# Performance work log

Measured on AMD Instinct MI355X. Metric: run time of the kernel, lower is better.

The kernel has to match this reference:

```python
import jax, jax.numpy as jnp
import numpy as np

H = W = 2048
TANH_C = 1.1486328125  # probability-correction constant from the model
DEG2RAD = np.float32(np.pi / 180.0)

# Fire-spread direction angle (degrees, East=0, counterclockwise) from the
# neighbor at 3x3 window position (r, c) toward the center cell.
DIR_DEG = jnp.array([[315., 270., 225.],
                     [  0.,   0., 180.],
                     [ 45.,  90., 135.]], dtype=jnp.float32)
CENTER_MASK = jnp.ones((3, 3), jnp.float32).at[1, 1].set(0.0)  # exclude self


def _neighborhood(x):
    """x: [H,W] -> [H,W,3,3] with [i,j,r,c] = x[i+r-1, j+c-1], zero padded."""
    xp = jnp.pad(x, 1)
    return jnp.stack(
        [jnp.stack([xp[r:r + H, c:c + W] for c in range(3)], axis=-1)
         for r in range(3)], axis=-2)


def setup_inputs() -> dict:
    key = jax.random.key(0)
    ks = jax.random.split(key, 8)
    p_veg = jax.random.uniform(ks[0], (H, W), jnp.float32)
    p_den = jax.random.uniform(ks[1], (H, W), jnp.float32)
    wind_velocity = jax.random.uniform(ks[2], (H, W), jnp.float32) * 10.0
    wind_towards_direction = jax.random.uniform(ks[3], (H, W), jnp.float32) * 360.0
    slope = (jax.random.uniform(ks[4], (H, W, 3, 3), jnp.float32) - 0.5) * 60.0
    burning = jax.random.uniform(ks[5], (H, W)) < 0.01  # sparse initial ignition
    burned = jnp.zeros((H, W), dtype=bool)
    rand_ignite = jax.random.uniform(ks[6], (H, W), jnp.float32)
    rand_continue = jax.random.uniform(ks[7], (H, W), jnp.float32)
    return dict(
        p_veg=p_veg, p_den=p_den,
        wind_velocity=wind_velocity, wind_towards_direction=wind_towards_direction,
        slope=slope,
        a=jnp.float32(0.1), p_h=jnp.float32(0.3),
        c_1=jnp.float32(0.1), c_2=jnp.float32(0.1), p_continue=jnp.float32(0.3),
        rand_ignite=rand_ignite, rand_continue=rand_continue,
        burning=burning, burned=burned,
    )


def reference(p_veg, p_den, wind_velocity, wind_towards_direction, slope,
              a, p_h, c_1, c_2, p_continue,
              rand_ignite, rand_continue, burning, burned):
    # p_w = exp(c1*V) * exp(c2*V*(cos(theta_w)-1)), theta_w = angle between
    # wind direction and per-neighbor spread direction. [H,W,3,3]
    theta_w = (wind_towards_direction[..., None, None] - DIR_DEG) * DEG2RAD
    p_w = (jnp.exp(c_1 * wind_velocity)[..., None, None]
           * jnp.exp(c_2 * wind_velocity[..., None, None] * (jnp.cos(theta_w) - 1.0)))
    # p_s = exp(a * theta_s), slope angle in radians. [H,W,3,3]
    p_s = jnp.exp(a * slope * DEG2RAD)
    # p_propagate = tanh(c * p_h*(1+p_veg)*(1+p_den)*p_w*p_s)
    p_base = p_h * (1.0 + p_veg) * (1.0 + p_den)  # [H,W]
    p_prop = jnp.tanh(TANH_C * (p_base[..., None, None] * p_w * p_s))
    # 8-neighbor burning indicators (center masked out). [H,W,3,3]
    nbr_burning = _neighborhood(burning.astype(jnp.float32)) * CENTER_MASK
    # p_ignite = 1 - prod_j (1 - p_propagate_j * burning_j)
    p_ignite = 1.0 - jnp.prod(1.0 - p_prop * nbr_burning, axis=(-2, -1))
    # Stochastic state transition.
    burnable = ~burning & ~burned
    new_ignited = burnable & (rand_ignite < p_ignite)
    keep = burning & (rand_continue < p_continue)
    new_burning = new_ignited | keep
    new_burned = burned | (burning & ~keep)
    return p_ignite, jnp.stack([new_burning, new_burned])
```

## Files before the change

kernel.cpp:

```cpp
#include <hip/hip_runtime.h>
#include <math.h>

namespace {

constexpr int H = 2048;
constexpr int W = 2048;
constexpr int HW = H * W;
constexpr float TANH_C  = 1.1486328125f;
constexpr float DEG2RAD = 0.017453292519943295f;
constexpr float RT2H    = 0.70710678118654752f;
constexpr float LOG2E   = 1.4426950408889634f;
constexpr float TWOPI   = 6.283185307179586f;

__device__ __forceinline__ float fexp2(float x) {
#if __has_builtin(__builtin_amdgcn_exp2f)
    return __builtin_amdgcn_exp2f(x);
#else
    return __exp2f(x);
#endif
}
__device__ __forceinline__ float fcos_rev(float x) {
#if __has_builtin(__builtin_amdgcn_cosf)
    return __builtin_amdgcn_cosf(x);
#else
    return __cosf(x * TWOPI);
#endif
}
__device__ __forceinline__ float fsin_rev(float x) {
#if __has_builtin(__builtin_amdgcn_sinf)
    return __builtin_amdgcn_sinf(x);
#else
    return __sinf(x * TWOPI);
#endif
}
__device__ __forceinline__ float frcp(float x) {
#if __has_builtin(__builtin_amdgcn_rcpf)
    return __builtin_amdgcn_rcpf(x);
#else
    return 1.0f / x;
#endif
}

__global__ __launch_bounds__(256) void wildfire_step(
    const float* __restrict__ p_veg,  const float* __restrict__ p_den,
    const float* __restrict__ wind_v, const float* __restrict__ wind_d,
    const float* __restrict__ slope,
    const float* __restrict__ s_a,  const float* __restrict__ s_ph,
    const float* __restrict__ s_c1, const float* __restrict__ s_c2,
    const float* __restrict__ s_pc,
    const float* __restrict__ rand_ig, const float* __restrict__ rand_co,
    const int* __restrict__ burning, const int* __restrict__ burned,
    float* __restrict__ out)
{
    __shared__ __align__(16) float sb[3][1032];
    __shared__ __align__(16) float pig_lds[1024];
    __shared__ unsigned short q[1024];
    __shared__ int qn;

    const int t  = (int)threadIdx.x;
    const int i  = (int)blockIdx.y;
    const int j0 = (int)blockIdx.x * 1024;
    const int rowbase = i * W + j0;

    if (t == 0) qn = 0;

    for (int r = 0; r < 3; ++r) {
        const int ii = i + r - 1;
        const bool rowok = (ii >= 0) && (ii < H);
        int4 v = make_int4(0, 0, 0, 0);
        if (rowok)
            v = *reinterpret_cast<const int4*>(burning + ii * W + j0 + 4 * t);
        float4 f;
        f.x = v.x ? 1.f : 0.f;  f.y = v.y ? 1.f : 0.f;
        f.z = v.z ? 1.f : 0.f;  f.w = v.w ? 1.f : 0.f;
        *reinterpret_cast<float4*>(&sb[r][4 + 4 * t]) = f;
        if (t == 0)
            sb[r][3] = (rowok && j0 > 0) ?
                       (burning[ii * W + j0 - 1] ? 1.f : 0.f) : 0.f;
        if (t == 1)
            sb[r][4 + 1024] = (rowok && j0 + 1024 < W) ?
                       (burning[ii * W + j0 + 1024] ? 1.f : 0.f) : 0.f;
    }
    __syncthreads();

    const int jb = t * 4;
    const int idx = rowbase + jb;

    float r0[6], r1[6], r2[6];
    {
        const float4 a = *reinterpret_cast<const float4*>(&sb[0][4 + jb]);
        const float4 b = *reinterpret_cast<const float4*>(&sb[1][4 + jb]);
        const float4 c = *reinterpret_cast<const float4*>(&sb[2][4 + jb]);
        r0[0] = sb[0][3 + jb]; r0[1] = a.x; r0[2] = a.y; r0[3] = a.z; r0[4] = a.w; r0[5] = sb[0][8 + jb];
        r1[0] = sb[1][3 + jb]; r1[1] = b.x; r1[2] = b.y; r1[3] = b.z; r1[4] = b.w; r1[5] = sb[1][8 + jb];
        r2[0] = sb[2][3 + jb]; r2[1] = c.x; r2[2] = c.y; r2[3] = c.z; r2[4] = c.w; r2[5] = sb[2][8 + jb];
    }

    float anyn[4];
    bool  isb[4];
#pragma unroll
    for (int x = 0; x < 4; ++x) {
        anyn[x] = ((r0[x] + r0[x+1]) + (r0[x+2] + r1[x]))
                + ((r1[x+2] + r2[x]) + (r2[x+1] + r2[x+2]));
        isb[x]  = (r1[x+1] != 0.f);
        if (anyn[x] != 0.f) {
            const int pos = atomicAdd(&qn, 1);
            q[pos] = (unsigned short)(jb + x);
        }
    }
    *reinterpret_cast<float4*>(&pig_lds[jb]) = make_float4(0.f, 0.f, 0.f, 0.f);
    __syncthreads();

    const int n = qn;
    for (int k = t; k < n; k += 256) {
        const int cell = (int)q[k];
        const int c    = 4 + cell;
        const float b0 = sb[0][c-1], b1 = sb[0][c], b2 = sb[0][c+1];
        const float b3 = sb[1][c-1],                b5 = sb[1][c+1];
        const float b6 = sb[2][c-1], b7 = sb[2][c], b8 = sb[2][c+1];
        const float cnt = ((b0 + b1) + (b2 + b3)) + ((b5 + b6) + (b7 + b8));

        const int gidx = rowbase + cell;
        const float pv = p_veg[gidx];
        const float pd = p_den[gidx];
        const float wv = wind_v[gidx];
        const float wd = wind_d[gidx];
        float sl[9];
        __builtin_memcpy(sl, slope + (size_t)gidx * 9, 9 * sizeof(float));

        const float a_  = s_a[0];
        const float p_h = s_ph[0];
        const float c1  = s_c1[0];
        const float c2  = s_c2[0];

        const float wrev = wd * (1.f / 360.f);
        const float cw = fcos_rev(wrev);
        const float sw = fsin_rev(wrev);

        const float Lc2wv = (LOG2E * c2) * wv;
        const float cwv = Lc2wv * cw, swv = Lc2wv * sw;
        const float cwr = RT2H * cwv, swr = RT2H * swv;
        const float dpl = cwr + swr;
        const float dmi = cwr - swr;
        const float aslL = (a_ * DEG2RAD) * LOG2E;
        const float p_base = (p_h * (1.f + pv)) * (1.f + pd);
        const float Cz2 = (2.f * LOG2E * TANH_C) * p_base
                        * fexp2(LOG2E * (c1 * wv - c2 * wv));

#define NEIGHBOR(K, b, T, sv)                                            \
        const float q##K = fmaf(aslL, (sv), (T));                        \
        const float z##K = Cz2 * fexp2(q##K);                            \
        const float E##K = fexp2(z##K);                                  \
        const float d##K = fmaf((b), E##K, 1.f);

        NEIGHBOR(0, b0,  dmi, sl[0])
        NEIGHBOR(1, b1, -swv, sl[1])
        NEIGHBOR(2, b2, -dpl, sl[2])
        NEIGHBOR(3, b3,  cwv, sl[3])
        NEIGHBOR(5, b5, -cwv, sl[5])
        NEIGHBOR(6, b6,  dpl, sl[6])
        NEIGHBOR(7, b7,  swv, sl[7])
        NEIGHBOR(8, b8, -dmi, sl[8])
#undef NEIGHBOR
        const float den = ((d0 * d1) * (d2 * d3)) * ((d5 * d6) * (d7 * d8));
        const float num = fexp2(cnt);
        pig_lds[cell] = fmaf(-num, frcp(den), 1.f);
    }
    __syncthreads();

    const int4  burned4 = *reinterpret_cast<const int4*>(burned + idx);
    const int   bn[4]   = {burned4.x, burned4.y, burned4.z, burned4.w};
    const float p_cont  = s_pc[0];

    const float4 pig4 = *reinterpret_cast<const float4*>(&pig_lds[jb]);
    const float pig[4] = {pig4.x, pig4.y, pig4.z, pig4.w};

    float rc[4] = {1.f, 1.f, 1.f, 1.f};
    if (isb[0] || isb[1] || isb[2] || isb[3]) {
        const float4 rco4 = *reinterpret_cast<const float4*>(rand_co + idx);
        rc[0] = rco4.x; rc[1] = rco4.y; rc[2] = rco4.z; rc[3] = rco4.w;
    }
    float rig[4] = {1.f, 1.f, 1.f, 1.f};
    if ((anyn[0] + anyn[1]) + (anyn[2] + anyn[3]) != 0.f) {
        const float4 rig4 = *reinterpret_cast<const float4*>(rand_ig + idx);
        rig[0] = rig4.x; rig[1] = rig4.y; rig[2] = rig4.z; rig[3] = rig4.w;
    }

    float4 o0, o1, o2;
    float* o0p = &o0.x; float* o1p = &o1.x; float* o2p = &o2.x;
#pragma unroll
    for (int x = 0; x < 4; ++x) {
        const bool ni   = (!isb[x]) && (bn[x] == 0) && (rig[x] < pig[x]);
        const bool keep = isb[x] && (rc[x] < p_cont);
        const bool nb   = ni || keep;
        const bool nd   = (bn[x] != 0) || (isb[x] && !keep);
        o0p[x] = pig[x];
        o1p[x] = nb ? 1.f : 0.f;
        o2p[x] = nd ? 1.f : 0.f;
    }
    *reinterpret_cast<float4*>(out + idx)          = o0;
    *reinterpret_cast<float4*>(out + HW + idx)     = o1;
    *reinterpret_cast<float4*>(out + 2 * HW + idx) = o2;
}

}

extern "C" void kernel_launch(void* const* d_in, const int* in_sizes, int n_in,
                              void* d_out, int out_size, void* d_ws, size_t ws_size,
                              hipStream_t stream)
{
    (void)in_sizes; (void)n_in; (void)out_size; (void)d_ws; (void)ws_size;
    dim3 grid(W / 1024, H, 1);
    dim3 block(256, 1, 1);
    hipLaunchKernelGGL(wildfire_step, grid, block, 0, stream,
        (const float*)d_in[0],  (const float*)d_in[1],
        (const float*)d_in[2],  (const float*)d_in[3],
        (const float*)d_in[4],
        (const float*)d_in[5],  (const float*)d_in[6],
        (const float*)d_in[7],  (const float*)d_in[8],
        (const float*)d_in[9],
        (const float*)d_in[10], (const float*)d_in[11],
        (const int*)d_in[12],   (const int*)d_in[13],
        (float*)d_out);
}
```

Baseline: 305.2 us.

## Split into dense state-transition kernel and sparse heavy ignition kernel

Splits the single kernel into two launches. A dense elementwise kernel writes zero p_ignite, the keep flag and the burned state for every cell. A second kernel recomputes the burning neighbourhood, evaluates the probability only for cells with burning neighbours and scatters p_ignite and new-ignition flags directly. This drops the LDS staging buffer and the extra barrier in the heavy path, but unconditionally reads rand_continue and writes all outputs twice for the affected cells, and it adds a second launch.

```diff
diff --git a/kernel.cpp b/kernel.cpp
--- a/kernel.cpp
+++ b/kernel.cpp
@@ -41,19 +41,47 @@
 #endif
 }
 
-__global__ __launch_bounds__(256) void wildfire_step(
+__global__ __launch_bounds__(256) void wildfire_dense(
+    const float* __restrict__ rand_co,
+    const int* __restrict__ burning, const int* __restrict__ burned,
+    const float* __restrict__ s_pc,
+    float* __restrict__ out)
+{
+    const int idx = ((int)blockIdx.x * 256 + (int)threadIdx.x) * 4;
+    const int4   b4  = *reinterpret_cast<const int4*>(burning + idx);
+    const int4   bd4 = *reinterpret_cast<const int4*>(burned + idx);
+    const float4 rc4 = *reinterpret_cast<const float4*>(rand_co + idx);
+    const float  p_cont = s_pc[0];
+
+    const int   bn[4] = {b4.x, b4.y, b4.z, b4.w};
+    const int   bd[4] = {bd4.x, bd4.y, bd4.z, bd4.w};
+    const float rc[4] = {rc4.x, rc4.y, rc4.z, rc4.w};
+
+    float4 o1, o2;
+    float* o1p = &o1.x; float* o2p = &o2.x;
+#pragma unroll
+    for (int x = 0; x < 4; ++x) {
+        const bool isb  = (bn[x] != 0);
+        const bool keep = isb && (rc[x] < p_cont);
+        o1p[x] = keep ? 1.f : 0.f;
+        o2p[x] = ((bd[x] != 0) || (isb && !keep)) ? 1.f : 0.f;
+    }
+    *reinterpret_cast<float4*>(out + idx)          = make_float4(0.f, 0.f, 0.f, 0.f);
+    *reinterpret_cast<float4*>(out + HW + idx)     = o1;
+    *reinterpret_cast<float4*>(out + 2 * HW + idx) = o2;
+}
+
+__global__ __launch_bounds__(256) void wildfire_heavy(
     const float* __restrict__ p_veg,  const float* __restrict__ p_den,
     const float* __restrict__ wind_v, const float* __restrict__ wind_d,
     const float* __restrict__ slope,
     const float* __restrict__ s_a,  const float* __restrict__ s_ph,
     const float* __restrict__ s_c1, const float* __restrict__ s_c2,
-    const float* __restrict__ s_pc,
-    const float* __restrict__ rand_ig, const float* __restrict__ rand_co,
+    const float* __restrict__ rand_ig,
     const int* __restrict__ burning, const int* __restrict__ burned,
     float* __restrict__ out)
 {
     __shared__ __align__(16) float sb[3][1032];
-    __shared__ __align__(16) float pig_lds[1024];
     __shared__ unsigned short q[1024];
     __shared__ int qn;
 
@@ -84,54 +112,50 @@
     __syncthreads();
 
     const int jb = t * 4;
-    const int idx = rowbase + jb;
-
-    float r0[6], r1[6], r2[6];
     {
         const float4 a = *reinterpret_cast<const float4*>(&sb[0][4 + jb]);
         const float4 b = *reinterpret_cast<const float4*>(&sb[1][4 + jb]);
         const float4 c = *reinterpret_cast<const float4*>(&sb[2][4 + jb]);
-        r0[0] = sb[0][3 + jb]; r0[1] = a.x; r0[2] = a.y; r0[3] = a.z; r0[4] = a.w; r0[5] = sb[0][8 + jb];
-        r1[0] = sb[1][3 + jb]; r1[1] = b.x; r1[2] = b.y; r1[3] = b.z; r1[4] = b.w; r1[5] = sb[1][8 + jb];
-        r2[0] = sb[2][3 + jb]; r2[1] = c.x; r2[2] = c.y; r2[3] = c.z; r2[4] = c.w; r2[5] = sb[2][8 + jb];
-    }
-
-    float anyn[4];
-    bool  isb[4];
+        const float r0[6] = {sb[0][3 + jb], a.x, a.y, a.z, a.w, sb[0][8 + jb]};
+        const float r1[6] = {sb[1][3 + jb], b.x, b.y, b.z, b.w, sb[1][8 + jb]};
+        const float r2[6] = {sb[2][3 + jb], c.x, c.y, c.z, c.w, sb[2][8 + jb]};
 #pragma unroll
-    for (int x = 0; x < 4; ++x) {
-        anyn[x] = ((r0[x] + r0[x+1]) + (r0[x+2] + r1[x]))
-                + ((r1[x+2] + r2[x]) + (r2[x+1] + r2[x+2]));
-        isb[x]  = (r1[x+1] != 0.f);
-        if (anyn[x] != 0.f) {
-            const int pos = atomicAdd(&qn, 1);
-            q[pos] = (unsigned short)(jb + x);
+        for (int x = 0; x < 4; ++x) {
+            const float anyn = ((r0[x] + r0[x+1]) + (r0[x+2] + r1[x]))
+                             + ((r1[x+2] + r2[x]) + (r2[x+1] + r2[x+2]));
+            if (anyn != 0.f) {
+                const int pos = atomicAdd(&qn, 1);
+                q[pos] = (unsigned short)(jb + x);
+            }
         }
     }
-    *reinterpret_cast<float4*>(&pig_lds[jb]) = make_float4(0.f, 0.f, 0.f, 0.f);
     __syncthreads();
 
     const int n = qn;
+    const float a_  = s_a[0];
+    const float p_h = s_ph[0];
+    const float c1  = s_c1[0];
+    const float c2  = s_c2[0];
+    const float aslL = (a_ * DEG2RAD) * LOG2E;
+
     for (int k = t; k < n; k += 256) {
         const int cell = (int)q[k];
         const int c    = 4 + cell;
+        const int gidx = rowbase + cell;
+
+        const float pv  = p_veg[gidx];
+        const float pd  = p_den[gidx];
+        const float wv  = wind_v[gidx];
+        const float wd  = wind_d[gidx];
+        const float rig = rand_ig[gidx];
+        const int   bn  = burned[gidx];
+        float sl[9];
+        __builtin_memcpy(sl, slope + (size_t)gidx * 9, 9 * sizeof(float));
+
         const float b0 = sb[0][c-1], b1 = sb[0][c], b2 = sb[0][c+1];
-        const float b3 = sb[1][c-1],                b5 = sb[1][c+1];
+        const float b3 = sb[1][c-1], bcn = sb[1][c], b5 = sb[1][c+1];
         const float b6 = sb[2][c-1], b7 = sb[2][c], b8 = sb[2][c+1];
         const float cnt = ((b0 + b1) + (b2 + b3)) + ((b5 + b6) + (b7 + b8));
-
-        const int gidx = rowbase + cell;
-        const float pv = p_veg[gidx];
-        const float pd = p_den[gidx];
-        const float wv = wind_v[gidx];
-        const float wd = wind_d[gidx];
-        float sl[9];
-        __builtin_memcpy(sl, slope + (size_t)gidx * 9, 9 * sizeof(float));
-
-        const float a_  = s_a[0];
-        const float p_h = s_ph[0];
-        const float c1  = s_c1[0];
-        const float c2  = s_c2[0];
 
         const float wrev = wd * (1.f / 360.f);
         const float cw = fcos_rev(wrev);
@@ -142,7 +166,6 @@
         const float cwr = RT2H * cwv, swr = RT2H * swv;
         const float dpl = cwr + swr;
         const float dmi = cwr - swr;
-        const float aslL = (a_ * DEG2RAD) * LOG2E;
         const float p_base = (p_h * (1.f + pv)) * (1.f + pd);
         const float Cz2 = (2.f * LOG2E * TANH_C) * p_base
                         * fexp2(LOG2E * (c1 * wv - c2 * wv));
@@ -164,43 +187,12 @@
 #undef NEIGHBOR
         const float den = ((d0 * d1) * (d2 * d3)) * ((d5 * d6) * (d7 * d8));
         const float num = fexp2(cnt);
-        pig_lds[cell] = fmaf(-num, frcp(den), 1.f);
-    }
-    __syncthreads();
-
-    const int4  burned4 = *reinterpret_cast<const int4*>(burned + idx);
-    const int   bn[4]   = {burned4.x, burned4.y, burned4.z, burned4.w};
-    const float p_cont  = s_pc[0];
-
-    const float4 pig4 = *reinterpret_cast<const float4*>(&pig_lds[jb]);
-    const float pig[4] = {pig4.x, pig4.y, pig4.z, pig4.w};
-
-    float rc[4] = {1.f, 1.f, 1.f, 1.f};
-    if (isb[0] || isb[1] || isb[2] || isb[3]) {
-        const float4 rco4 = *reinterpret_cast<const float4*>(rand_co + idx);
-        rc[0] = rco4.x; rc[1] = rco4.y; rc[2] = rco4.z; rc[3] = rco4.w;
-    }
-    float rig[4] = {1.f, 1.f, 1.f, 1.f};
-    if ((anyn[0] + anyn[1]) + (anyn[2] + anyn[3]) != 0.f) {
-        const float4 rig4 = *reinterpret_cast<const float4*>(rand_ig + idx);
-        rig[0] = rig4.x; rig[1] = rig4.y; rig[2] = rig4.z; rig[3] = rig4.w;
-    }
-
-    float4 o0, o1, o2;
-    float* o0p = &o0.x; float* o1p = &o1.x; float* o2p = &o2.x;
-#pragma unroll
-    for (int x = 0; x < 4; ++x) {
-        const bool ni   = (!isb[x]) && (bn[x] == 0) && (rig[x] < pig[x]);
-        const bool keep = isb[x] && (rc[x] < p_cont);
-        const bool nb   = ni || keep;
-        const bool nd   = (bn[x] != 0) || (isb[x] && !keep);
-        o0p[x] = pig[x];
-        o1p[x] = nb ? 1.f : 0.f;
-        o2p[x] = nd ? 1.f : 0.f;
-    }
-    *reinterpret_cast<float4*>(out + idx)          = o0;
-    *reinterpret_cast<float4*>(out + HW + idx)     = o1;
-    *reinterpret_cast<float4*>(out + 2 * HW + idx) = o2;
+        const float pig = fmaf(-num, frcp(den), 1.f);
+
+        out[gidx] = pig;
+        const bool ni = (bcn == 0.f) && (bn == 0) && (rig < pig);
+        if (ni) out[HW + gidx] = 1.f;
+    }
 }
 
 }
@@ -210,16 +202,28 @@
                               hipStream_t stream)
 {
     (void)in_sizes; (void)n_in; (void)out_size; (void)d_ws; (void)ws_size;
-    dim3 grid(W / 1024, H, 1);
-    dim3 block(256, 1, 1);
-    hipLaunchKernelGGL(wildfire_step, grid, block, 0, stream,
-        (const float*)d_in[0],  (const float*)d_in[1],
-        (const float*)d_in[2],  (const float*)d_in[3],
-        (const float*)d_in[4],
-        (const float*)d_in[5],  (const float*)d_in[6],
-        (const float*)d_in[7],  (const float*)d_in[8],
-        (const float*)d_in[9],
-        (const float*)d_in[10], (const float*)d_in[11],
-        (const int*)d_in[12],   (const int*)d_in[13],
-        (float*)d_out);
-}
+
+    {
+        dim3 grid(HW / 1024, 1, 1);
+        dim3 block(256, 1, 1);
+        hipLaunchKernelGGL(wildfire_dense, grid, block, 0, stream,
+            (const float*)d_in[11],
+            (const int*)d_in[12],
+            (const int*)d_in[13],
+            (const float*)d_in[9],
+            (float*)d_out);
+    }
+    {
+        dim3 grid(W / 1024, H, 1);
+        dim3 block(256, 1, 1);
+        hipLaunchKernelGGL(wildfire_heavy, grid, block, 0, stream,
+            (const float*)d_in[0],  (const float*)d_in[1],
+            (const float*)d_in[2],  (const float*)d_in[3],
+            (const float*)d_in[4],
+            (const float*)d_in[5],  (const float*)d_in[6],
+            (const float*)d_in[7],  (const float*)d_in[8],
+            (const float*)d_in[10],
+            (const int*)d_in[12],   (const int*)d_in[13],
+            (float*)d_out);
+    }
+}
```

Result: no change. 311.3 us (+2.0%).
